# Performance work log

Measured on AMD Instinct MI355X. Metric: run time of the kernel, lower is better.

The kernel has to match this reference:

```python
import jax, jax.numpy as jnp
import numpy as np

B, L, D_MODEL, H, HD, FD = 1, 1024, 1024, 16, 64, 64
EPS = 1e-12

def setup_inputs() -> dict:
    key = jax.random.key(0)
    ks = jax.random.split(key, 7)
    s = 1.0 / np.sqrt(D_MODEL)
    return {
        'x': jax.random.normal(ks[0], (B, L, D_MODEL), jnp.float32),
        'Wq': jax.random.normal(ks[1], (D_MODEL, H * HD), jnp.float32) * s,
        'Wk': jax.random.normal(ks[2], (D_MODEL, H * HD), jnp.float32) * s,
        'Wv': jax.random.normal(ks[3], (D_MODEL, H * HD), jnp.float32) * s,
        'Wo': jax.random.normal(ks[4], (H * HD, D_MODEL), jnp.float32) * s,
        'Kq': jax.random.normal(ks[5], (H, HD, FD), jnp.float32) * (1.0 / np.sqrt(HD)),
        'Kk': jax.random.normal(ks[6], (H, HD, FD), jnp.float32) * (1.0 / np.sqrt(HD)),
    }

def _heads(t):
    # (b, l, h*d) -> (b, h, l, d)
    b, l, _ = t.shape
    return t.reshape(b, l, H, HD).transpose(0, 2, 1, 3)

def _feature_map(t, K):
    # UntiedHeadEinsumMLP (no skip) + SoftmaxDim with temp=1.0
    f = jnp.einsum('hdf,bhld->bhlf', K, t)
    feats = jnp.concatenate([jax.nn.softmax(f, axis=-1), jax.nn.softmax(-f, axis=-1)], axis=-1)
    return jnp.maximum(feats, EPS)  # clamp(min=eps)

def reference(x, Wq, Wk, Wv, Wo, Kq, Kk):
    q = _heads(x @ Wq)  # b h l d
    k = _heads(x @ Wk)
    v = _heads(x @ Wv)
    qf = _feature_map(q, Kq)  # b h l 2f
    kf = _feature_map(k, Kk)  # b h l 2f
    # causal linear attention: o_t = phi(q_t) . sum_{s<=t} phi(k_s) v_s^T, normalized
    kv = jnp.cumsum(kf[:, :, :, None, :] * v[..., None], axis=2)  # b h l d 2f
    o = jnp.einsum('bhlf,bhldf->bhld', qf, kv)
    z = jnp.einsum('bhlf,bhlf->bhl', qf, jnp.cumsum(kf, axis=2)) + EPS
    o = o / z[..., None]
    y = o.transpose(0, 2, 1, 3).reshape(x.shape[0], x.shape[1], H * HD)
    return y @ Wo
```

## Files before the change

kernel.cpp:

```cpp
#include <hip/hip_runtime.h>
#include <hip/hip_bf16.h>


#define NH 16
#define NC 16

using short8 = __attribute__((ext_vector_type(8))) short;
using f32x4  = __attribute__((ext_vector_type(4))) float;
typedef const __attribute__((address_space(1))) char* gptr1;
typedef __attribute__((address_space(3))) char* lptr3;

static __device__ __forceinline__ unsigned short bf16bits(float x) {
    __hip_bfloat16 h = __float2bfloat16(x);
    return __builtin_bit_cast(unsigned short, h);
}
static __device__ __forceinline__ float b2f(unsigned short u) {
    return __builtin_bit_cast(float, (unsigned int)u << 16);
}
#define SWZ(row, cb) ((cb) ^ (((row) & 7) << 4))

template<int RS>
static __device__ __forceinline__ short8 ldfrag(const char* buf, int row, int kelem) {
    return *(const short8*)(buf + row * RS + SWZ(row, kelem * 2));
}

__global__ __launch_bounds__(256) void prep(const float* __restrict__ x,
                                            const float* __restrict__ w0,
                                            const float* __restrict__ w1,
                                            const float* __restrict__ w2,
                                            const float* __restrict__ w3,
                                            const float* __restrict__ Kq,
                                            const float* __restrict__ Kk,
                                            __hip_bfloat16* __restrict__ xb,
                                            __hip_bfloat16* __restrict__ d0,
                                            __hip_bfloat16* __restrict__ d1,
                                            __hip_bfloat16* __restrict__ d2,
                                            __hip_bfloat16* __restrict__ d3,
                                            __hip_bfloat16* __restrict__ KqT,
                                            __hip_bfloat16* __restrict__ KkT) {
    const int z = blockIdx.z;
    const int tid = threadIdx.x;
    if (z < 4) {
        const float* src = (z == 0) ? w0 : (z == 1) ? w1 : (z == 2) ? w2 : w3;
        __hip_bfloat16* dst = (z == 0) ? d0 : (z == 1) ? d1 : (z == 2) ? d2 : d3;
        __shared__ float tile[64][68];
        const int bx = blockIdx.x * 64, by = blockIdx.y * 64;
#pragma unroll
        for (int j = 0; j < 4; j++) {
            const int idx = j * 256 + tid;
            const int kr = idx >> 4, c4 = idx & 15;
            float4 v = *(const float4*)&src[(size_t)(by + kr) * 1024 + bx + c4 * 4];
            *(float4*)&tile[kr][c4 * 4] = v;
        }
        __syncthreads();
        const int n = tid >> 2, k0 = (tid & 3) * 16;
        unsigned short* drow = (unsigned short*)dst + (size_t)(bx + n) * 1024 + by + k0;
#pragma unroll
        for (int q = 0; q < 4; q++) {
            ushort4 o;
            o.x = bf16bits(tile[k0 + q * 4 + 0][n]);
            o.y = bf16bits(tile[k0 + q * 4 + 1][n]);
            o.z = bf16bits(tile[k0 + q * 4 + 2][n]);
            o.w = bf16bits(tile[k0 + q * 4 + 3][n]);
            *(ushort4*)(drow + q * 4) = o;
        }
    } else if (z == 4) {
        const int blk = blockIdx.y * 16 + blockIdx.x;
#pragma unroll
        for (int j = 0; j < 4; j++) {
            const int i = blk * 4096 + j * 1024 + tid * 4;
            float4 v = *(const float4*)(x + i);
            ushort4 o;
            o.x = bf16bits(v.x); o.y = bf16bits(v.y); o.z = bf16bits(v.z); o.w = bf16bits(v.w);
            *(ushort4*)((unsigned short*)xb + i) = o;
        }
    } else {
        const int flat = blockIdx.y * 16 + blockIdx.x;
        if (flat >= 32) return;
        const int h = flat & 15;
        const float* S = (flat >> 4) ? Kk : Kq;
        __hip_bfloat16* D = (flat >> 4) ? KkT : KqT;
        __shared__ float t[64][65];
#pragma unroll
        for (int j = 0; j < 16; j++) {
            int e = tid + j * 256, r = e >> 6, c = e & 63;
            t[r][c] = S[h * 4096 + r * 64 + c];
        }
        __syncthreads();
#pragma unroll
        for (int j = 0; j < 16; j++) {
            int e = tid + j * 256, r = e >> 6, c = e & 63;
            D[h * 4096 + r * 64 + c] = __float2bfloat16(t[c][r]);
        }
    }
}

__global__ __launch_bounds__(256) void qkv_feat(const __hip_bfloat16* __restrict__ A,
                                                const __hip_bfloat16* __restrict__ B0,
                                                const __hip_bfloat16* __restrict__ B1,
                                                const __hip_bfloat16* __restrict__ B2,
                                                const __hip_bfloat16* __restrict__ KqT,
                                                const __hip_bfloat16* __restrict__ KkT,
                                                __hip_bfloat16* __restrict__ qf,
                                                __hip_bfloat16* __restrict__ kf,
                                                __hip_bfloat16* __restrict__ kfT,
                                                __hip_bfloat16* __restrict__ VT) {
    __shared__ __align__(16) char smem[49152];
    const int tid = threadIdx.x;
    const int bm = blockIdx.y * 128;
    const int which = blockIdx.x >> 4;
    const int h = blockIdx.x & 15;
    const __hip_bfloat16* B = (which == 0) ? B0 : (which == 1) ? B1 : B2;
    const int bn = h * 64;
    const int wid = tid >> 6, lane = tid & 63;
    const int g = lane >> 4, r16 = lane & 15;
    const char* Ab = (const char*)A;
    const char* Bb = (const char*)B;
    f32x4 acc[2][4] = {};

#define QKV_STAGE(dstA, dstB, kbyte)                                                                   \
    do {                                                                                               \
        _Pragma("unroll") for (int it = 0; it < 4; it++) {                                             \
            const int off = it * 4096 + tid * 16;                                                      \
            const int row = off >> 7, cb = off & 127;                                                  \
            __builtin_amdgcn_global_load_lds((gptr1)(Ab + (size_t)(bm + row) * 2048 + (kbyte) + SWZ(row, cb)), \
                                             (lptr3)((dstA) + it * 4096 + wid * 1024), 16, 0, 0);      \
        }                                                                                              \
        _Pragma("unroll") for (int it = 0; it < 2; it++) {                                             \
            const int off = it * 4096 + tid * 16;                                                      \
            const int row = off >> 7, cb = off & 127;                                                  \
            __builtin_amdgcn_global_load_lds((gptr1)(Bb + (size_t)(bn + row) * 2048 + (kbyte) + SWZ(row, cb)), \
                                             (lptr3)((dstB) + it * 4096 + wid * 1024), 16, 0, 0);      \
        }                                                                                              \
    } while (0)

    QKV_STAGE(smem, smem + 32768, 0);
    for (int kt = 0; kt < 16; kt++) {
        char* Ac = smem + ((kt & 1) ? 16384 : 0);
        char* Bc = smem + 32768 + ((kt & 1) ? 8192 : 0);
        if (kt < 15) {
            char* An = smem + ((kt & 1) ? 0 : 16384);
            char* Bn = smem + 32768 + ((kt & 1) ? 0 : 8192);
            QKV_STAGE(An, Bn, (kt + 1) * 128);
            asm volatile("s_waitcnt vmcnt(6)" ::: "memory");
        } else {
            asm volatile("s_waitcnt vmcnt(0)" ::: "memory");
        }
        __builtin_amdgcn_s_barrier();
#pragma unroll
        for (int ks = 0; ks < 2; ks++) {
            short8 af[2], bfr[4];
#pragma unroll
            for (int m = 0; m < 2; m++)
                af[m] = ldfrag<128>(Ac, wid * 32 + m * 16 + r16, ks * 32 + g * 8);
#pragma unroll
            for (int n = 0; n < 4; n++)
                bfr[n] = ldfrag<128>(Bc, n * 16 + r16, ks * 32 + g * 8);
#pragma unroll
            for (int m = 0; m < 2; m++)
#pragma unroll
// ... 37 lines not shown
        for (int it = 0; it < 2; it++) {
            const int off = it * 4096 + tid * 16;
            const int row = off >> 7, cb = off & 127;
            __builtin_amdgcn_global_load_lds((gptr1)(KTp + (size_t)(h * 64 + row) * 128 + SWZ(row, cb)),
                                             (lptr3)(smem + it * 4096 + wid * 1024), 16, 0, 0);
        }
    }
    __syncthreads();

    f32x4 fr[2][4] = {};
#pragma unroll
    for (int ks = 0; ks < 2; ks++) {
        short8 af[2], bfr[4];
#pragma unroll
        for (int m = 0; m < 2; m++)
            af[m] = ldfrag<128>(XS, wid * 32 + m * 16 + r16, ks * 32 + g * 8);
#pragma unroll
        for (int n = 0; n < 4; n++)
            bfr[n] = ldfrag<128>(smem, n * 16 + r16, ks * 32 + g * 8);
#pragma unroll
        for (int m = 0; m < 2; m++)
#pragma unroll
            for (int n = 0; n < 4; n++)
                fr[m][n] = __builtin_amdgcn_mfma_f32_16x16x32_bf16(af[m], bfr[n], fr[m][n], 0, 0, 0);
    }
    if (kside) __syncthreads();

    char* ft = smem;
    __hip_bfloat16* feat = kside ? kf : qf;
#pragma unroll
    for (int m = 0; m < 2; m++)
#pragma unroll
        for (int i = 0; i < 4; i++) {
            const int row = wid * 32 + m * 16 + g * 4 + i;
            float m1 = fr[m][0][i], m2 = -fr[m][0][i];
#pragma unroll
            for (int n = 1; n < 4; n++) {
                m1 = fmaxf(m1, fr[m][n][i]);
                m2 = fmaxf(m2, -fr[m][n][i]);
            }
#pragma unroll
            for (int off = 8; off; off >>= 1) {
                m1 = fmaxf(m1, __shfl_xor(m1, off));
                m2 = fmaxf(m2, __shfl_xor(m2, off));
            }
            float e1[4], e2[4], s1 = 0.f, s2 = 0.f;
#pragma unroll
            for (int n = 0; n < 4; n++) {
                e1[n] = __expf(fr[m][n][i] - m1);  s1 += e1[n];
                e2[n] = __expf(-fr[m][n][i] - m2); s2 += e2[n];
            }
#pragma unroll
            for (int off = 8; off; off >>= 1) {
                s1 += __shfl_xor(s1, off);
                s2 += __shfl_xor(s2, off);
            }
            const float i1 = 1.f / s1, i2 = 1.f / s2;
            __hip_bfloat16* fo = feat + ((size_t)(h * 1024 + bm + row)) * 128;
#pragma unroll
            for (int n = 0; n < 4; n++) {
                const int col = n * 16 + r16;
                unsigned short v1 = bf16bits(fmaxf(e1[n] * i1, 1e-12f));
                unsigned short v2 = bf16bits(fmaxf(e2[n] * i2, 1e-12f));
                *(unsigned short*)(fo + col) = v1;
                *(unsigned short*)(fo + col + 64) = v2;
                if (kside) {
                    *(unsigned short*)(ft + col * 256 + SWZ(col, row * 2)) = v1;
                    *(unsigned short*)(ft + (col + 64) * 256 + SWZ(col + 64, row * 2)) = v2;
                }
            }
        }
    if (kside) {
        __syncthreads();
#pragma unroll
        for (int j = 0; j < 8; j++) {
            const int off = (tid + j * 256) * 16;
            const int row = off >> 8, cb = off & 255;
            short8 v = *(const short8*)(ft + row * 256 + SWZ(row, cb));
            *(short8*)((char*)kfT + ((size_t)(h * 128 + row) * 1024 + bm) * 2 + cb) = v;
        }
    }
}

__global__ __launch_bounds__(256) void chunk_sums_mfma(const __hip_bfloat16* __restrict__ kfT,
                                                       const __hip_bfloat16* __restrict__ VT,
                                                       __hip_bfloat16* __restrict__ Scb,
                                                       float* __restrict__ ksum) {
    const int h = blockIdx.y, c = blockIdx.x, l0 = c * 64;
    __shared__ __align__(16) char VTs[64 * 128];
    __shared__ __align__(16) char KTs[128 * 128];
    const int tid = threadIdx.x, lane = tid & 63, wid = tid >> 6;
    const int r16 = lane & 15, g = lane >> 4;
#pragma unroll
    for (int it = 0; it < 2; it++) {
        const int off = it * 4096 + tid * 16;
        const int row = off >> 7, cb = off & 127;
        __builtin_amdgcn_global_load_lds((gptr1)((const char*)VT + ((size_t)(h * 64 + row) * 1024 + l0) * 2 + SWZ(row, cb)),
                                         (lptr3)(VTs + it * 4096 + wid * 1024), 16, 0, 0);
    }
#pragma unroll
    for (int it = 0; it < 4; it++) {
        const int off = it * 4096 + tid * 16;
        const int row = off >> 7, cb = off & 127;
        __builtin_amdgcn_global_load_lds((gptr1)((const char*)kfT + ((size_t)(h * 128 + row) * 1024 + l0) * 2 + SWZ(row, cb)),
                                         (lptr3)(KTs + it * 4096 + wid * 1024), 16, 0, 0);
    }
    __syncthreads();
    f32x4 acc[8] = {};
#pragma unroll
    for (int ks = 0; ks < 2; ks++) {
        short8 a = ldfrag<128>(VTs, wid * 16 + r16, ks * 32 + g * 8);
#pragma unroll
        for (int n = 0; n < 8; n++) {
            short8 b = ldfrag<128>(KTs, n * 16 + r16, ks * 32 + g * 8);
            acc[n] = __builtin_amdgcn_mfma_f32_16x16x32_bf16(a, b, acc[n], 0, 0, 0);
        }
    }
    unsigned short* o = (unsigned short*)Scb + (size_t)(h * NC + c) * 8192;
#pragma unroll
    for (int n = 0; n < 8; n++)
#pragma unroll
        for (int i = 0; i < 4; i++)
            o[(wid * 16 + g * 4 + i) * 128 + n * 16 + r16] = bf16bits(acc[n][i]);
    if (tid < 128) {
        float s = 0.f;
#pragma unroll 8
        for (int t = 0; t < 64; t++)
            s += b2f(*(const unsigned short*)(KTs + tid * 128 + SWZ(tid, t * 2)));
        ksum[(size_t)(h * NC + c) * 128 + tid] = s;
    }
}

__global__ __launch_bounds__(256) void prefix_scan(const __hip_bfloat16* __restrict__ Scb,
                                                   __hip_bfloat16* __restrict__ Sp,
                                                   const float* __restrict__ ksum,
                                                   float* __restrict__ kp) {
    const int h = blockIdx.x, eb = blockIdx.y, tid = threadIdx.x;
#pragma unroll
    for (int j = 0; j < 4; j++) {
        const int e = eb * 1024 + tid + j * 256;
        float v[NC];
#pragma unroll
        for (int c = 0; c < NC; c++)
            v[c] = b2f(((const unsigned short*)Scb)[(size_t)(h * NC + c) * 8192 + e]);
        float run = 0.f;
#pragma unroll
        for (int c = 0; c < NC; c++) {
            Sp[(size_t)(h * NC + c) * 8192 + e] = __float2bfloat16(run);
            run += v[c];
        }
    }
    if (eb == 0 && tid < 128) {
        float run = 0.f;
#pragma unroll
        for (int c = 0; c < NC; c++) {
            const size_t idx = (size_t)(h * NC + c) * 128 + tid;
            kp[idx] = run;
            run += ksum[idx];
        }
    }
}

__global__ __launch_bounds__(256) void chunk_out_mfma(const __hip_bfloat16* __restrict__ qf,
                                                      const __hip_bfloat16* __restrict__ kf,
                                                      const __hip_bfloat16* __restrict__ VT,
                                                      const __hip_bfloat16* __restrict__ Sp,
                                                      const float* __restrict__ kp,
                                                      __hip_bfloat16* __restrict__ Y) {
    const int h = blockIdx.y, c = blockIdx.x, l0 = c * 64;
    __shared__ __align__(16) char QF[64 * 256];
    __shared__ __align__(16) char KF[64 * 256];
    __shared__ __align__(16) char SP[64 * 256];
    __shared__ __align__(16) char VTs[64 * 128];
    __shared__ __align__(16) char AM[64 * 128];
    __shared__ float zi[64];
    __shared__ float invz[64];
    const int tid = threadIdx.x, lane = tid & 63, wid = tid >> 6;
    const int r16 = lane & 15, g = lane >> 4;

#pragma unroll
    for (int it = 0; it < 4; it++) {
        const int off = it * 4096 + wid * 1024 + lane * 16;
        const int row = off >> 8, cb = off & 255;
        const int sw = SWZ(row, cb);
        __builtin_amdgcn_global_load_lds((gptr1)((const char*)qf + ((size_t)(h * 1024 + l0 + row)) * 256 + sw),
                                         (lptr3)(QF + it * 4096 + wid * 1024), 16, 0, 0);
        __builtin_amdgcn_global_load_lds((gptr1)((const char*)kf + ((size_t)(h * 1024 + l0 + row)) * 256 + sw),
                                         (lptr3)(KF + it * 4096 + wid * 1024), 16, 0, 0);
        __builtin_amdgcn_global_load_lds((gptr1)((const char*)Sp + ((size_t)((h * NC + c) * 64 + row)) * 256 + sw),
                                         (lptr3)(SP + it * 4096 + wid * 1024), 16, 0, 0);
    }
#pragma unroll
    for (int it = 0; it < 2; it++) {
        const int off = it * 4096 + wid * 1024 + lane * 16;
        const int row = off >> 7, cb = off & 127;
        __builtin_amdgcn_global_load_lds((gptr1)((const char*)VT + ((size_t)(h * 64 + row) * 1024 + l0) * 2 + SWZ(row, cb)),
                                         (lptr3)(VTs + it * 4096 + wid * 1024), 16, 0, 0);
    }
    __syncthreads();

    f32x4 a4[4] = {};
#pragma unroll
    for (int ks = 0; ks < 4; ks++) {
        short8 a = ldfrag<256>(QF, wid * 16 + r16, ks * 32 + g * 8);
#pragma unroll
        for (int n = 0; n < 4; n++) {
            short8 bb = ldfrag<256>(KF, n * 16 + r16, ks * 32 + g * 8);
            a4[n] = __builtin_amdgcn_mfma_f32_16x16x32_bf16(a, bb, a4[n], 0, 0, 0);
        }
    }
    const int rowl = wid * 16 + g * 4;
#pragma unroll
    for (int i = 0; i < 4; i++) {
        float r = 0.f;
#pragma unroll
        for (int n = 0; n < 4; n++) {
            const int col = n * 16 + r16;
            float v = (col <= rowl + i) ? a4[n][i] : 0.f;
            a4[n][i] = v;
            r += v;
        }
#pragma unroll
        for (int off = 8; off; off >>= 1) r += __shfl_xor(r, off);
        if (r16 == 0) zi[rowl + i] = r;
#pragma unroll
        for (int n = 0; n < 4; n++)
            *(unsigned short*)(AM + (rowl + i) * 128 + SWZ(rowl + i, (n * 16 + r16) * 2)) = bf16bits(a4[n][i]);
    }
    __syncthreads();

    if (tid < 64) {
        float z = zi[tid] + 1e-12f;
        const float* kpp = kp + (size_t)(h * NC + c) * 128;
#pragma unroll 8
        for (int f = 0; f < 128; f++)
            z += b2f(*(const unsigned short*)(QF + tid * 256 + SWZ(tid, f * 2))) * kpp[f];
        invz[tid] = 1.f / z;
    }

    f32x4 o4[4] = {};
#pragma unroll
    for (int ks = 0; ks < 2; ks++) {
        short8 a = ldfrag<128>(AM, wid * 16 + r16, ks * 32 + g * 8);
#pragma unroll
        for (int n = 0; n < 4; n++) {
            short8 bb = ldfrag<128>(VTs, n * 16 + r16, ks * 32 + g * 8);
            o4[n] = __builtin_amdgcn_mfma_f32_16x16x32_bf16(a, bb, o4[n], 0, 0, 0);
        }
    }
#pragma unroll
    for (int ks = 0; ks < 4; ks++) {
        short8 a = ldfrag<256>(QF, wid * 16 + r16, ks * 32 + g * 8);
#pragma unroll
        for (int n = 0; n < 4; n++) {
            short8 bb = ldfrag<256>(SP, n * 16 + r16, ks * 32 + g * 8);
            o4[n] = __builtin_amdgcn_mfma_f32_16x16x32_bf16(a, bb, o4[n], 0, 0, 0);
        }
    }
    __syncthreads();
#pragma unroll
    for (int n = 0; n < 4; n++)
#pragma unroll
        for (int i = 0; i < 4; i++) {
            const int row = rowl + i, col = n * 16 + r16;
            Y[((size_t)(l0 + row)) * 1024 + h * 64 + col] = __float2bfloat16(o4[n][i] * invz[row]);
        }
}

__global__ __launch_bounds__(256) void gemm_final(const __hip_bfloat16* __restrict__ A,
                                                  const __hip_bfloat16* __restrict__ B,
                                                  float* __restrict__ C) {
    __shared__ __align__(16) char smem[32768];
    const int tid = threadIdx.x;
    const int bm = blockIdx.y * 64, bn = blockIdx.x * 64;
    const int wid = tid >> 6, lane = tid & 63;
    const int g = lane >> 4, r16 = lane & 15;
    const int wr = wid >> 1, wc = wid & 1;
    const char* Ab = (const char*)A;
    const char* Bb = (const char*)B;
    f32x4 acc[2][2] = {};

#define FIN_STAGE(dstA, dstB, kbyte)                                                                   \
    do {                                                                                               \
        _Pragma("unroll") for (int it = 0; it < 2; it++) {                                             \
            const int off = it * 4096 + tid * 16;                                                      \
            const int row = off >> 7, cb = off & 127;                                                  \
            __builtin_amdgcn_global_load_lds((gptr1)(Ab + (size_t)(bm + row) * 2048 + (kbyte) + SWZ(row, cb)), \
                                             (lptr3)((dstA) + it * 4096 + wid * 1024), 16, 0, 0);      \
            __builtin_amdgcn_global_load_lds((gptr1)(Bb + (size_t)(bn + row) * 2048 + (kbyte) + SWZ(row, cb)), \
                                             (lptr3)((dstB) + it * 4096 + wid * 1024), 16, 0, 0);      \
        }                                                                                              \
    } while (0)

    FIN_STAGE(smem, smem + 16384, 0);
    for (int kt = 0; kt < 16; kt++) {
        char* Ac = smem + ((kt & 1) ? 8192 : 0);
        char* Bc = smem + 16384 + ((kt & 1) ? 8192 : 0);
        if (kt < 15) {
            char* An = smem + ((kt & 1) ? 0 : 8192);
            char* Bn = smem + 16384 + ((kt & 1) ? 0 : 8192);
            FIN_STAGE(An, Bn, (kt + 1) * 128);
            asm volatile("s_waitcnt vmcnt(4)" ::: "memory");
        } else {
            asm volatile("s_waitcnt vmcnt(0)" ::: "memory");
        }
        __builtin_amdgcn_s_barrier();
#pragma unroll
        for (int ks = 0; ks < 2; ks++) {
            short8 af[2], bfr[2];
#pragma unroll
            for (int m = 0; m < 2; m++)
                af[m] = ldfrag<128>(Ac, wr * 32 + m * 16 + r16, ks * 32 + g * 8);
#pragma unroll
            for (int n = 0; n < 2; n++)
                bfr[n] = ldfrag<128>(Bc, wc * 32 + n * 16 + r16, ks * 32 + g * 8);
#pragma unroll
            for (int m = 0; m < 2; m++)
#pragma unroll
                for (int n = 0; n < 2; n++)
                    acc[m][n] = __builtin_amdgcn_mfma_f32_16x16x32_bf16(af[m], bfr[n], acc[m][n], 0, 0, 0);
        }
        asm volatile("s_waitcnt lgkmcnt(0)" ::: "memory");
        __builtin_amdgcn_s_barrier();
    }
#undef FIN_STAGE
#pragma unroll
    for (int m = 0; m < 2; m++)
#pragma unroll
        for (int n = 0; n < 2; n++)
#pragma unroll
            for (int i = 0; i < 4; i++) {
                const int row = bm + wr * 32 + m * 16 + g * 4 + i;
                const int col = bn + wc * 32 + n * 16 + r16;
                C[(size_t)row * 1024 + col] = acc[m][n][i];
            }
}

extern "C" void kernel_launch(void* const* d_in, const int* in_sizes, int n_in,
                              void* d_out, int out_size, void* d_ws, size_t ws_size,
                              hipStream_t stream) {
    const float* x  = (const float*)d_in[0];
    const float* Wq = (const float*)d_in[1];
    const float* Wk = (const float*)d_in[2];
    const float* Wv = (const float*)d_in[3];
    const float* Wo = (const float*)d_in[4];
    const float* Kq = (const float*)d_in[5];
    const float* Kk = (const float*)d_in[6];
    float* out = (float*)d_out;
    float* ws = (float*)d_ws;

    const size_t M1 = 1024 * 1024;
    if (ws_size < 10 * M1 * sizeof(float)) return;

    __hip_bfloat16* xb  = (__hip_bfloat16*)(ws);
    __hip_bfloat16* Wqt = (__hip_bfloat16*)(ws + M1 / 2);
    __hip_bfloat16* Wkt = (__hip_bfloat16*)(ws + 1 * M1);
    __hip_bfloat16* Wvt = (__hip_bfloat16*)(ws + 3 * M1 / 2);
    __hip_bfloat16* Wot = (__hip_bfloat16*)(ws + 2 * M1);
    __hip_bfloat16* KqT = (__hip_bfloat16*)(ws + 5 * M1 / 2);
    __hip_bfloat16* KkT = (__hip_bfloat16*)(ws + 5 * M1 / 2 + 32768);
    __hip_bfloat16* VT  = (__hip_bfloat16*)(ws + 3 * M1);
    __hip_bfloat16* qfb = (__hip_bfloat16*)(ws + 7 * M1 / 2);
    __hip_bfloat16* kfb = (__hip_bfloat16*)(ws + 9 * M1 / 2);
    __hip_bfloat16* kfT = (__hip_bfloat16*)(ws + 11 * M1 / 2);
    __hip_bfloat16* Scb = (__hip_bfloat16*)(ws + 13 * M1 / 2);
    __hip_bfloat16* Spb = (__hip_bfloat16*)(ws + 15 * M1 / 2);
    __hip_bfloat16* Yb  = (__hip_bfloat16*)(ws + 17 * M1 / 2);
    float* ksum = ws + 9 * M1;
    float* kp   = ws + 9 * M1 + 32768;

    prep<<<dim3(16, 16, 6), 256, 0, stream>>>(x, Wq, Wk, Wv, Wo, Kq, Kk,
                                              xb, Wqt, Wkt, Wvt, Wot, KqT, KkT);
    qkv_feat<<<dim3(48, 8), 256, 0, stream>>>(xb, Wqt, Wkt, Wvt, KqT, KkT, qfb, kfb, kfT, VT);
    chunk_sums_mfma<<<dim3(NC, NH), 256, 0, stream>>>(kfT, VT, Scb, ksum);
    prefix_scan<<<dim3(NH, 8), 256, 0, stream>>>(Scb, Spb, ksum, kp);
    chunk_out_mfma<<<dim3(NC, NH), 256, 0, stream>>>(qfb, kfb, VT, Spb, kp, Yb);
    gemm_final<<<dim3(16, 16), 256, 0, stream>>>(Yb, Wot, out);
}
```

Baseline: 54.83 us.

## Fuse chunk sums, prefix scan, chunk output and output GEMM into one flag-synchronized kernel

Replaces four tail kernels with a single persistent-style kernel that computes per-chunk KV sums, publishes them via release flags, and has each block sum all earlier chunks' states itself instead of a separate prefix scan. After writing Y, blocks wait on a per-row-chunk counter until all heads are done, then run the output projection tile for that chunk. This removes three launches and the Sp/kp intermediate round-trips, but adds spin-waits that rely on all 256 blocks being co-resident and repeats prefix summation work (quadratic in chunk count).

```diff
diff --git a/kernel.cpp b/kernel.cpp
--- a/kernel.cpp
+++ b/kernel.cpp
@@ -37,7 +37,8 @@
                                             __hip_bfloat16* __restrict__ d2,
                                             __hip_bfloat16* __restrict__ d3,
                                             __hip_bfloat16* __restrict__ KqT,
-                                            __hip_bfloat16* __restrict__ KkT) {
+                                            __hip_bfloat16* __restrict__ KkT,
+                                            int* __restrict__ flags) {
     const int z = blockIdx.z;
     const int tid = threadIdx.x;
     if (z < 4) {
@@ -76,6 +77,12 @@
         }
     } else {
         const int flat = blockIdx.y * 16 + blockIdx.x;
+        if (flat == 32) {
+            flags[tid] = 0;
+            if (tid < 16) flags[256 + tid] = 0;
+            return;
+        }
+        if (flat > 32) return;
         if (flat >= 32) return;
         const int h = flat & 15;
         const float* S = (flat >> 4) ? Kk : Kq;
@@ -279,101 +286,72 @@
     }
 }
 
-__global__ __launch_bounds__(256) void chunk_sums_mfma(const __hip_bfloat16* __restrict__ kfT,
-                                                       const __hip_bfloat16* __restrict__ VT,
-                                                       __hip_bfloat16* __restrict__ Scb,
-                                                       float* __restrict__ ksum) {
+__global__ __launch_bounds__(256) void tail_fused(const __hip_bfloat16* __restrict__ kfT,
+                                                  const __hip_bfloat16* __restrict__ VT,
+                                                  const __hip_bfloat16* __restrict__ qf,
+                                                  const __hip_bfloat16* __restrict__ kf,
+                                                  __hip_bfloat16* __restrict__ Scb,
+                                                  float* __restrict__ ksum,
+                                                  int* __restrict__ flags,
+                                                  __hip_bfloat16* __restrict__ Y,
+                                                  const __hip_bfloat16* __restrict__ Wot,
+                                                  float* __restrict__ out) {
+    __shared__ __align__(16) char smem[65536];
+    char* QF  = smem;
+    char* KF  = smem + 16384;
+    char* SP  = smem + 32768;
+    char* VTs = smem + 49152;
+    char* AM  = smem + 57344;
+    __shared__ float kpL[128];
+    __shared__ float zi[64], invz[64];
     const int h = blockIdx.y, c = blockIdx.x, l0 = c * 64;
-    __shared__ __align__(16) char VTs[64 * 128];
-    __shared__ __align__(16) char KTs[128 * 128];
     const int tid = threadIdx.x, lane = tid & 63, wid = tid >> 6;
     const int r16 = lane & 15, g = lane >> 4;
-#pragma unroll
-    for (int it = 0; it < 2; it++) {
-        const int off = it * 4096 + tid * 16;
-        const int row = off >> 7, cb = off & 127;
-        __builtin_amdgcn_global_load_lds((gptr1)((const char*)VT + ((size_t)(h * 64 + row) * 1024 + l0) * 2 + SWZ(row, cb)),
-                                         (lptr3)(VTs + it * 4096 + wid * 1024), 16, 0, 0);
-    }
-#pragma unroll
-    for (int it = 0; it < 4; it++) {
-        const int off = it * 4096 + tid * 16;
-        const int row = off >> 7, cb = off & 127;
-        __builtin_amdgcn_global_load_lds((gptr1)((const char*)kfT + ((size_t)(h * 128 + row) * 1024 + l0) * 2 + SWZ(row, cb)),
-                                         (lptr3)(KTs + it * 4096 + wid * 1024), 16, 0, 0);
+    int* flagsY = flags + 256;
+
+    {
+#pragma unroll
+        for (int it = 0; it < 2; it++) {
+            const int off = it * 4096 + tid * 16;
+            const int row = off >> 7, cb = off & 127;
+            __builtin_amdgcn_global_load_lds((gptr1)((const char*)VT + ((size_t)(h * 64 + row) * 1024 + l0) * 2 + SWZ(row, cb)),
+                                             (lptr3)(VTs + it * 4096 + wid * 1024), 16, 0, 0);
+        }
+#pragma unroll
+        for (int it = 0; it < 4; it++) {
+            const int off = it * 4096 + tid * 16;
+            const int row = off >> 7, cb = off & 127;
+            __builtin_amdgcn_global_load_lds((gptr1)((const char*)kfT + ((size_t)(h * 128 + row) * 1024 + l0) * 2 + SWZ(row, cb)),
+                                             (lptr3)(KF + it * 4096 + wid * 1024), 16, 0, 0);
+        }
+        __syncthreads();
+        f32x4 acc[8] = {};
+#pragma unroll
+        for (int ks = 0; ks < 2; ks++) {
+            short8 a = ldfrag<128>(VTs, wid * 16 + r16, ks * 32 + g * 8);
+#pragma unroll
+            for (int n = 0; n < 8; n++) {
+                short8 bb = ldfrag<128>(KF, n * 16 + r16, ks * 32 + g * 8);
+                acc[n] = __builtin_amdgcn_mfma_f32_16x16x32_bf16(a, bb, acc[n], 0, 0, 0);
+            }
+        }
+        unsigned short* o = (unsigned short*)Scb + (size_t)(h * NC + c) * 8192;
+#pragma unroll
+        for (int n = 0; n < 8; n++)
+#pragma unroll
+            for (int i = 0; i < 4; i++)
+                o[(wid * 16 + g * 4 + i) * 128 + n * 16 + r16] = bf16bits(acc[n][i]);
+        if (tid < 128) {
+            float s = 0.f;
+#pragma unroll 8
+            for (int t = 0; t < 64; t++)
+                s += b2f(*(const unsigned short*)(KF + tid * 128 + SWZ(tid, t * 2)));
+            ksum[(size_t)(h * NC + c) * 128 + tid] = s;
+        }
     }
     __syncthreads();
-    f32x4 acc[8] = {};
-#pragma unroll
-    for (int ks = 0; ks < 2; ks++) {
-        short8 a = ldfrag<128>(VTs, wid * 16 + r16, ks * 32 + g * 8);
-#pragma unroll
-        for (int n = 0; n < 8; n++) {
-            short8 b = ldfrag<128>(KTs, n * 16 + r16, ks * 32 + g * 8);
-            acc[n] = __builtin_amdgcn_mfma_f32_16x16x32_bf16(a, b, acc[n], 0, 0, 0);
-        }
-    }
-    unsigned short* o = (unsigned short*)Scb + (size_t)(h * NC + c) * 8192;
-#pragma unroll
-    for (int n = 0; n < 8; n++)
-#pragma unroll
-        for (int i = 0; i < 4; i++)
-            o[(wid * 16 + g * 4 + i) * 128 + n * 16 + r16] = bf16bits(acc[n][i]);
-    if (tid < 128) {
-        float s = 0.f;
-#pragma unroll 8
-        for (int t = 0; t < 64; t++)
-            s += b2f(*(const unsigned short*)(KTs + tid * 128 + SWZ(tid, t * 2)));
-        ksum[(size_t)(h * NC + c) * 128 + tid] = s;
-    }
-}
-
-__global__ __launch_bounds__(256) void prefix_scan(const __hip_bfloat16* __restrict__ Scb,
-                                                   __hip_bfloat16* __restrict__ Sp,
-                                                   const float* __restrict__ ksum,
-                                                   float* __restrict__ kp) {
-    const int h = blockIdx.x, eb = blockIdx.y, tid = threadIdx.x;
-#pragma unroll
-    for (int j = 0; j < 4; j++) {
-        const int e = eb * 1024 + tid + j * 256;
-        float v[NC];
-#pragma unroll
-        for (int c = 0; c < NC; c++)
-            v[c] = b2f(((const unsigned short*)Scb)[(size_t)(h * NC + c) * 8192 + e]);
-        float run = 0.f;
-#pragma unroll
-        for (int c = 0; c < NC; c++) {
-            Sp[(size_t)(h * NC + c) * 8192 + e] = __float2bfloat16(run);
-            run += v[c];
-        }
-    }
-    if (eb == 0 && tid < 128) {
-        float run = 0.f;
-#pragma unroll
-        for (int c = 0; c < NC; c++) {
-            const size_t idx = (size_t)(h * NC + c) * 128 + tid;
-            kp[idx] = run;
-            run += ksum[idx];
-        }
-    }
-}
-
-__global__ __launch_bounds__(256) void chunk_out_mfma(const __hip_bfloat16* __restrict__ qf,
-                                                      const __hip_bfloat16* __restrict__ kf,
-                                                      const __hip_bfloat16* __restrict__ VT,
-                                                      const __hip_bfloat16* __restrict__ Sp,
-                                                      const float* __restrict__ kp,
-                                                      __hip_bfloat16* __restrict__ Y) {
-    const int h = blockIdx.y, c = blockIdx.x, l0 = c * 64;
-    __shared__ __align__(16) char QF[64 * 256];
-    __shared__ __align__(16) char KF[64 * 256];
-    __shared__ __align__(16) char SP[64 * 256];
-    __shared__ __align__(16) char VTs[64 * 128];
-    __shared__ __align__(16) char AM[64 * 128];
-    __shared__ float zi[64];
-    __shared__ float invz[64];
-    const int tid = threadIdx.x, lane = tid & 63, wid = tid >> 6;
-    const int r16 = lane & 15, g = lane >> 4;
+    if (tid == 0)
+        __hip_atomic_store(&flags[h * NC + c], 1, __ATOMIC_RELEASE, __HIP_MEMORY_SCOPE_AGENT);
 
 #pragma unroll
     for (int it = 0; it < 4; it++) {
@@ -384,98 +362,123 @@
                                          (lptr3)(QF + it * 4096 + wid * 1024), 16, 0, 0);
         __builtin_amdgcn_global_load_lds((gptr1)((const char*)kf + ((size_t)(h * 1024 + l0 + row)) * 256 + sw),
                                          (lptr3)(KF + it * 4096 + wid * 1024), 16, 0, 0);
-        __builtin_amdgcn_global_load_lds((gptr1)((const char*)Sp + ((size_t)((h * NC + c) * 64 + row)) * 256 + sw),
-                                         (lptr3)(SP + it * 4096 + wid * 1024), 16, 0, 0);
-    }
-#pragma unroll
-    for (int it = 0; it < 2; it++) {
-        const int off = it * 4096 + wid * 1024 + lane * 16;
-        const int row = off >> 7, cb = off & 127;
-        __builtin_amdgcn_global_load_lds((gptr1)((const char*)VT + ((size_t)(h * 64 + row) * 1024 + l0) * 2 + SWZ(row, cb)),
-                                         (lptr3)(VTs + it * 4096 + wid * 1024), 16, 0, 0);
-    }
+    }
+
+    if (tid < c)
+        while (__hip_atomic_load(&flags[h * NC + tid], __ATOMIC_ACQUIRE, __HIP_MEMORY_SCOPE_AGENT) == 0) {}
     __syncthreads();
 
-    f32x4 a4[4] = {};
-#pragma unroll
-    for (int ks = 0; ks < 4; ks++) {
-        short8 a = ldfrag<256>(QF, wid * 16 + r16, ks * 32 + g * 8);
-#pragma unroll
-        for (int n = 0; n < 4; n++) {
-            short8 bb = ldfrag<256>(KF, n * 16 + r16, ks * 32 + g * 8);
-            a4[n] = __builtin_amdgcn_mfma_f32_16x16x32_bf16(a, bb, a4[n], 0, 0, 0);
-        }
-    }
-    const int rowl = wid * 16 + g * 4;
-#pragma unroll
-    for (int i = 0; i < 4; i++) {
-        float r = 0.f;
-#pragma unroll
-        for (int n = 0; n < 4; n++) {
-            const int col = n * 16 + r16;
-            float v = (col <= rowl + i) ? a4[n][i] : 0.f;
-            a4[n][i] = v;
-            r += v;
-        }
-#pragma unroll
-        for (int off = 8; off; off >>= 1) r += __shfl_xor(r, off);
-        if (r16 == 0) zi[rowl + i] = r;
+    {
+        const int e0 = tid * 32;
+        const int d = e0 >> 7, f0 = e0 & 127;
+        float a[32];
+#pragma unroll
+        for (int j = 0; j < 32; j++) a[j] = 0.f;
+        for (int cp = 0; cp < c; cp++) {
+            const unsigned short* p = (const unsigned short*)Scb + (size_t)(h * NC + cp) * 8192 + e0;
+#pragma unroll
+            for (int q = 0; q < 4; q++) {
+                short8 v = *(const short8*)(p + q * 8);
+#pragma unroll
+                for (int j = 0; j < 8; j++) a[q * 8 + j] += b2f((unsigned short)v[j]);
+            }
+        }
+#pragma unroll
+        for (int q = 0; q < 4; q++) {
+            short8 w;
+#pragma unroll
+            for (int j = 0; j < 8; j++) w[j] = (short)bf16bits(a[q * 8 + j]);
+            *(short8*)(SP + d * 256 + SWZ(d, (f0 + q * 8) * 2)) = w;
+        }
+        if (tid < 128) {
+            float s = 0.f;
+            for (int cp = 0; cp < c; cp++)
+                s += ksum[(size_t)(h * NC + cp) * 128 + tid];
+            kpL[tid] = s;
+        }
+    }
+    __syncthreads();
+
+    {
+        f32x4 a4[4] = {};
+#pragma unroll
+        for (int ks = 0; ks < 4; ks++) {
+            short8 a = ldfrag<256>(QF, wid * 16 + r16, ks * 32 + g * 8);
+#pragma unroll
+            for (int n = 0; n < 4; n++) {
+                short8 bb = ldfrag<256>(KF, n * 16 + r16, ks * 32 + g * 8);
+                a4[n] = __builtin_amdgcn_mfma_f32_16x16x32_bf16(a, bb, a4[n], 0, 0, 0);
+            }
+        }
+        const int rowl = wid * 16 + g * 4;
+#pragma unroll
+        for (int i = 0; i < 4; i++) {
+            float r = 0.f;
+#pragma unroll
+            for (int n = 0; n < 4; n++) {
+                const int col = n * 16 + r16;
+                float v = (col <= rowl + i) ? a4[n][i] : 0.f;
+                a4[n][i] = v;
+                r += v;
+            }
+#pragma unroll
+            for (int off = 8; off; off >>= 1) r += __shfl_xor(r, off);
+            if (r16 == 0) zi[rowl + i] = r;
+#pragma unroll
+            for (int n = 0; n < 4; n++)
+                *(unsigned short*)(AM + (rowl + i) * 128 + SWZ(rowl + i, (n * 16 + r16) * 2)) = bf16bits(a4[n][i]);
+        }
+        __syncthreads();
+
+        if (tid < 64) {
+            float z = zi[tid] + 1e-12f;
+#pragma unroll 8
+            for (int f = 0; f < 128; f++)
+                z += b2f(*(const unsigned short*)(QF + tid * 256 + SWZ(tid, f * 2))) * kpL[f];
+            invz[tid] = 1.f / z;
+        }
+
+        f32x4 o4[4] = {};
+#pragma unroll
+        for (int ks = 0; ks < 2; ks++) {
+            short8 a = ldfrag<128>(AM, wid * 16 + r16, ks * 32 + g * 8);
+#pragma unroll
+            for (int n = 0; n < 4; n++) {
+                short8 bb = ldfrag<128>(VTs, n * 16 + r16, ks * 32 + g * 8);
+                o4[n] = __builtin_amdgcn_mfma_f32_16x16x32_bf16(a, bb, o4[n], 0, 0, 0);
+            }
+        }
+#pragma unroll
+        for (int ks = 0; ks < 4; ks++) {
+            short8 a = ldfrag<256>(QF, wid * 16 + r16, ks * 32 + g * 8);
+#pragma unroll
+            for (int n = 0; n < 4; n++) {
+                short8 bb = ldfrag<256>(SP, n * 16 + r16, ks * 32 + g * 8);
+                o4[n] = __builtin_amdgcn_mfma_f32_16x16x32_bf16(a, bb, o4[n], 0, 0, 0);
+            }
+        }
+        __syncthreads();
 #pragma unroll
         for (int n = 0; n < 4; n++)
-            *(unsigned short*)(AM + (rowl + i) * 128 + SWZ(rowl + i, (n * 16 + r16) * 2)) = bf16bits(a4[n][i]);
+#pragma unroll
+            for (int i = 0; i < 4; i++) {
+                const int row = rowl + i, col = n * 16 + r16;
+                Y[((size_t)(l0 + row)) * 1024 + h * 64 + col] = __float2bfloat16(o4[n][i] * invz[row]);
+            }
     }
     __syncthreads();
-
-    if (tid < 64) {
-        float z = zi[tid] + 1e-12f;
-        const float* kpp = kp + (size_t)(h * NC + c) * 128;
-#pragma unroll 8
-        for (int f = 0; f < 128; f++)
-            z += b2f(*(const unsigned short*)(QF + tid * 256 + SWZ(tid, f * 2))) * kpp[f];
-        invz[tid] = 1.f / z;
-    }
-
-    f32x4 o4[4] = {};
-#pragma unroll
-    for (int ks = 0; ks < 2; ks++) {
-        short8 a = ldfrag<128>(AM, wid * 16 + r16, ks * 32 + g * 8);
-#pragma unroll
-        for (int n = 0; n < 4; n++) {
-            short8 bb = ldfrag<128>(VTs, n * 16 + r16, ks * 32 + g * 8);
-            o4[n] = __builtin_amdgcn_mfma_f32_16x16x32_bf16(a, bb, o4[n], 0, 0, 0);
-        }
-    }
-#pragma unroll
-    for (int ks = 0; ks < 4; ks++) {
-        short8 a = ldfrag<256>(QF, wid * 16 + r16, ks * 32 + g * 8);
-#pragma unroll
-        for (int n = 0; n < 4; n++) {
-            short8 bb = ldfrag<256>(SP, n * 16 + r16, ks * 32 + g * 8);
-            o4[n] = __builtin_amdgcn_mfma_f32_16x16x32_bf16(a, bb, o4[n], 0, 0, 0);
-        }
+    if (tid == 0) {
+        __hip_atomic_fetch_add(&flagsY[c], 1, __ATOMIC_RELEASE, __HIP_MEMORY_SCOPE_AGENT);
+        while (__hip_atomic_load(&flagsY[c], __ATOMIC_ACQUIRE, __HIP_MEMORY_SCOPE_AGENT) < NH) {}
     }
     __syncthreads();
-#pragma unroll
-    for (int n = 0; n < 4; n++)
-#pragma unroll
-        for (int i = 0; i < 4; i++) {
-            const int row = rowl + i, col = n * 16 + r16;
-            Y[((size_t)(l0 + row)) * 1024 + h * 64 + col] = __float2bfloat16(o4[n][i] * invz[row]);
-        }
-}
-
-__global__ __launch_bounds__(256) void gemm_final(const __hip_bfloat16* __restrict__ A,
-                                                  const __hip_bfloat16* __restrict__ B,
-                                                  float* __restrict__ C) {
-    __shared__ __align__(16) char smem[32768];
-    const int tid = threadIdx.x;
-    const int bm = blockIdx.y * 64, bn = blockIdx.x * 64;
-    const int wid = tid >> 6, lane = tid & 63;
-    const int g = lane >> 4, r16 = lane & 15;
-    const int wr = wid >> 1, wc = wid & 1;
-    const char* Ab = (const char*)A;
-    const char* Bb = (const char*)B;
-    f32x4 acc[2][2] = {};
+
+    {
+        const int bm = c * 64, bn = h * 64;
+        const int wr = wid >> 1, wc = wid & 1;
+        const char* Ab = (const char*)Y;
+        const char* Bb = (const char*)Wot;
+        f32x4 acc[2][2] = {};
 
 #define FIN_STAGE(dstA, dstB, kbyte)                                                                   \
     do {                                                                                               \
@@ -489,48 +492,49 @@
         }                                                                                              \
     } while (0)
 
-    FIN_STAGE(smem, smem + 16384, 0);
-    for (int kt = 0; kt < 16; kt++) {
-        char* Ac = smem + ((kt & 1) ? 8192 : 0);
-        char* Bc = smem + 16384 + ((kt & 1) ? 8192 : 0);
-        if (kt < 15) {
-            char* An = smem + ((kt & 1) ? 0 : 8192);
-            char* Bn = smem + 16384 + ((kt & 1) ? 0 : 8192);
-            FIN_STAGE(An, Bn, (kt + 1) * 128);
-            asm volatile("s_waitcnt vmcnt(4)" ::: "memory");
-        } else {
-            asm volatile("s_waitcnt vmcnt(0)" ::: "memory");
-        }
-        __builtin_amdgcn_s_barrier();
-#pragma unroll
-        for (int ks = 0; ks < 2; ks++) {
-            short8 af[2], bfr[2];
-#pragma unroll
-            for (int m = 0; m < 2; m++)
-                af[m] = ldfrag<128>(Ac, wr * 32 + m * 16 + r16, ks * 32 + g * 8);
+        FIN_STAGE(QF, KF, 0);
+        for (int kt = 0; kt < 16; kt++) {
+            char* Ac = QF + ((kt & 1) ? 8192 : 0);
+            char* Bc = KF + ((kt & 1) ? 8192 : 0);
+            if (kt < 15) {
+                char* An = QF + ((kt & 1) ? 0 : 8192);
+                char* Bn = KF + ((kt & 1) ? 0 : 8192);
+                FIN_STAGE(An, Bn, (kt + 1) * 128);
+                asm volatile("s_waitcnt vmcnt(4)" ::: "memory");
+            } else {
+                asm volatile("s_waitcnt vmcnt(0)" ::: "memory");
+            }
+            __builtin_amdgcn_s_barrier();
+#pragma unroll
+            for (int ks = 0; ks < 2; ks++) {
+                short8 af[2], bfr[2];
+#pragma unroll
+                for (int m = 0; m < 2; m++)
+                    af[m] = ldfrag<128>(Ac, wr * 32 + m * 16 + r16, ks * 32 + g * 8);
+#pragma unroll
+                for (int n = 0; n < 2; n++)
+                    bfr[n] = ldfrag<128>(Bc, wc * 32 + n * 16 + r16, ks * 32 + g * 8);
+#pragma unroll
+                for (int m = 0; m < 2; m++)
+#pragma unroll
+                    for (int n = 0; n < 2; n++)
+                        acc[m][n] = __builtin_amdgcn_mfma_f32_16x16x32_bf16(af[m], bfr[n], acc[m][n], 0, 0, 0);
+            }
+            asm volatile("s_waitcnt lgkmcnt(0)" ::: "memory");
+            __builtin_amdgcn_s_barrier();
+        }
+#undef FIN_STAGE
+#pragma unroll
+        for (int m = 0; m < 2; m++)
 #pragma unroll
             for (int n = 0; n < 2; n++)
-                bfr[n] = ldfrag<128>(Bc, wc * 32 + n * 16 + r16, ks * 32 + g * 8);
-#pragma unroll
-            for (int m = 0; m < 2; m++)
-#pragma unroll
-                for (int n = 0; n < 2; n++)
-                    acc[m][n] = __builtin_amdgcn_mfma_f32_16x16x32_bf16(af[m], bfr[n], acc[m][n], 0, 0, 0);
-        }
-        asm volatile("s_waitcnt lgkmcnt(0)" ::: "memory");
-        __builtin_amdgcn_s_barrier();
-    }
-#undef FIN_STAGE
-#pragma unroll
-    for (int m = 0; m < 2; m++)
-#pragma unroll
-        for (int n = 0; n < 2; n++)
-#pragma unroll
-            for (int i = 0; i < 4; i++) {
-                const int row = bm + wr * 32 + m * 16 + g * 4 + i;
-                const int col = bn + wc * 32 + n * 16 + r16;
-                C[(size_t)row * 1024 + col] = acc[m][n][i];
-            }
+#pragma unroll
+                for (int i = 0; i < 4; i++) {
+                    const int row = bm + wr * 32 + m * 16 + g * 4 + i;
+                    const int col = bn + wc * 32 + n * 16 + r16;
+                    out[(size_t)row * 1024 + col] = acc[m][n][i];
+                }
+    }
 }
 
 extern "C" void kernel_launch(void* const* d_in, const int* in_sizes, int n_in,
@@ -561,16 +565,12 @@
     __hip_bfloat16* kfb = (__hip_bfloat16*)(ws + 9 * M1 / 2);
     __hip_bfloat16* kfT = (__hip_bfloat16*)(ws + 11 * M1 / 2);
     __hip_bfloat16* Scb = (__hip_bfloat16*)(ws + 13 * M1 / 2);
-    __hip_bfloat16* Spb = (__hip_bfloat16*)(ws + 15 * M1 / 2);
-    __hip_bfloat16* Yb  = (__hip_bfloat16*)(ws + 17 * M1 / 2);
+    __hip_bfloat16* Yb  = (__hip_bfloat16*)(ws + 15 * M1 / 2);
     float* ksum = ws + 9 * M1;
-    float* kp   = ws + 9 * M1 + 32768;
+    int*   flags = (int*)(ws + 9 * M1 + 32768);
 
     prep<<<dim3(16, 16, 6), 256, 0, stream>>>(x, Wq, Wk, Wv, Wo, Kq, Kk,
-                                              xb, Wqt, Wkt, Wvt, Wot, KqT, KkT);
+                                              xb, Wqt, Wkt, Wvt, Wot, KqT, KkT, flags);
     qkv_feat<<<dim3(48, 8), 256, 0, stream>>>(xb, Wqt, Wkt, Wvt, KqT, KkT, qfb, kfb, kfT, VT);
-    chunk_sums_mfma<<<dim3(NC, NH), 256, 0, stream>>>(kfT, VT, Scb, ksum);
-    prefix_scan<<<dim3(NH, 8), 256, 0, stream>>>(Scb, Spb, ksum, kp);
-    chunk_out_mfma<<<dim3(NC, NH), 256, 0, stream>>>(qfb, kfb, VT, Spb, kp, Yb);
-    gemm_final<<<dim3(16, 16), 256, 0, stream>>>(Yb, Wot, out);
-}
+    tail_fused<<<dim3(NC, NH), 256, 0, stream>>>(kfT, VT, qfb, kfb, Scb, ksum, flags, Yb, Wot, out);
+}
```

Result: slower. 79.92 us (+45.8%).

## Fuse chunk state sums and prefix scan into one sequential pipelined kernel

Applied to the files above, without the earlier changes.

Replaces the per-chunk sum kernel and the separate prefix-scan kernel with a single kernel. Each block walks all chunks of a head sequentially, keeping the running state in registers and the running key sum in LDS, and double-buffers the next chunk's loads. This removes a kernel launch and the round trip of the per-chunk sums through global memory. In exchange the grid shrinks from 256 blocks to 32, and the chunk loop is serialized, which may leave most of the GPU idle.

```diff
diff --git a/kernel.cpp b/kernel.cpp
--- a/kernel.cpp
+++ b/kernel.cpp
@@ -279,83 +279,92 @@
     }
 }
 
-__global__ __launch_bounds__(256) void chunk_sums_mfma(const __hip_bfloat16* __restrict__ kfT,
-                                                       const __hip_bfloat16* __restrict__ VT,
-                                                       __hip_bfloat16* __restrict__ Scb,
-                                                       float* __restrict__ ksum) {
-    const int h = blockIdx.y, c = blockIdx.x, l0 = c * 64;
-    __shared__ __align__(16) char VTs[64 * 128];
-    __shared__ __align__(16) char KTs[128 * 128];
+__global__ __launch_bounds__(256) void chunk_scan(const __hip_bfloat16* __restrict__ kfT,
+                                                  const __hip_bfloat16* __restrict__ VT,
+                                                  __hip_bfloat16* __restrict__ Sp,
+                                                  float* __restrict__ kp) {
+    __shared__ __align__(16) char smem[40960];
+    __shared__ float kprun[128];
+    __shared__ float kpP[2][128];
+    const int h = blockIdx.y, dh = blockIdx.x;
     const int tid = threadIdx.x, lane = tid & 63, wid = tid >> 6;
     const int r16 = lane & 15, g = lane >> 4;
-#pragma unroll
-    for (int it = 0; it < 2; it++) {
-        const int off = it * 4096 + tid * 16;
-        const int row = off >> 7, cb = off & 127;
-        __builtin_amdgcn_global_load_lds((gptr1)((const char*)VT + ((size_t)(h * 64 + row) * 1024 + l0) * 2 + SWZ(row, cb)),
-                                         (lptr3)(VTs + it * 4096 + wid * 1024), 16, 0, 0);
-    }
-#pragma unroll
-    for (int it = 0; it < 4; it++) {
-        const int off = it * 4096 + tid * 16;
-        const int row = off >> 7, cb = off & 127;
-        __builtin_amdgcn_global_load_lds((gptr1)((const char*)kfT + ((size_t)(h * 128 + row) * 1024 + l0) * 2 + SWZ(row, cb)),
-                                         (lptr3)(KTs + it * 4096 + wid * 1024), 16, 0, 0);
-    }
-    __syncthreads();
-    f32x4 acc[8] = {};
-#pragma unroll
-    for (int ks = 0; ks < 2; ks++) {
-        short8 a = ldfrag<128>(VTs, wid * 16 + r16, ks * 32 + g * 8);
-#pragma unroll
-        for (int n = 0; n < 8; n++) {
-            short8 b = ldfrag<128>(KTs, n * 16 + r16, ks * 32 + g * 8);
-            acc[n] = __builtin_amdgcn_mfma_f32_16x16x32_bf16(a, b, acc[n], 0, 0, 0);
-        }
-    }
-    unsigned short* o = (unsigned short*)Scb + (size_t)(h * NC + c) * 8192;
-#pragma unroll
-    for (int n = 0; n < 8; n++)
-#pragma unroll
-        for (int i = 0; i < 4; i++)
-            o[(wid * 16 + g * 4 + i) * 128 + n * 16 + r16] = bf16bits(acc[n][i]);
-    if (tid < 128) {
-        float s = 0.f;
-#pragma unroll 8
-        for (int t = 0; t < 64; t++)
-            s += b2f(*(const unsigned short*)(KTs + tid * 128 + SWZ(tid, t * 2)));
-        ksum[(size_t)(h * NC + c) * 128 + tid] = s;
-    }
-}
-
-__global__ __launch_bounds__(256) void prefix_scan(const __hip_bfloat16* __restrict__ Scb,
-                                                   __hip_bfloat16* __restrict__ Sp,
-                                                   const float* __restrict__ ksum,
-                                                   float* __restrict__ kp) {
-    const int h = blockIdx.x, eb = blockIdx.y, tid = threadIdx.x;
-#pragma unroll
-    for (int j = 0; j < 4; j++) {
-        const int e = eb * 1024 + tid + j * 256;
-        float v[NC];
-#pragma unroll
-        for (int c = 0; c < NC; c++)
-            v[c] = b2f(((const unsigned short*)Scb)[(size_t)(h * NC + c) * 8192 + e]);
-        float run = 0.f;
-#pragma unroll
-        for (int c = 0; c < NC; c++) {
-            Sp[(size_t)(h * NC + c) * 8192 + e] = __float2bfloat16(run);
-            run += v[c];
-        }
-    }
-    if (eb == 0 && tid < 128) {
-        float run = 0.f;
-#pragma unroll
-        for (int c = 0; c < NC; c++) {
-            const size_t idx = (size_t)(h * NC + c) * 128 + tid;
-            kp[idx] = run;
-            run += ksum[idx];
-        }
-    }
+    if (tid < 128) kprun[tid] = 0.f;
+
+    f32x4 acc[2][2] = {};
+
+#define CS_STAGE(p, kc)                                                                                 \
+    do {                                                                                                \
+        char* bufp = smem + (p) * 20480;                                                                \
+        {                                                                                               \
+            const int off = tid * 16;                                                                   \
+            const int row = off >> 7, cb = off & 127;                                                   \
+            __builtin_amdgcn_global_load_lds((gptr1)((const char*)VT + ((size_t)(h * 64 + dh * 32 + row) * 1024 + (kc) * 64) * 2 + SWZ(row, cb)), \
+                                             (lptr3)(bufp + wid * 1024), 16, 0, 0);                     \
+        }                                                                                               \
+        _Pragma("unroll") for (int it = 0; it < 4; it++) {                                              \
+            const int off = it * 4096 + tid * 16;                                                       \
+            const int row = off >> 7, cb = off & 127;                                                   \
+            __builtin_amdgcn_global_load_lds((gptr1)((const char*)kfT + ((size_t)(h * 128 + row) * 1024 + (kc) * 64) * 2 + SWZ(row, cb)), \
+                                             (lptr3)(bufp + 4096 + it * 4096 + wid * 1024), 16, 0, 0);  \
+        }                                                                                               \
+    } while (0)
+
+    CS_STAGE(0, 0);
+    for (int c = 0; c < NC; c++) {
+        char* VTc = smem + (c & 1) * 20480;
+        char* KTc = VTc + 4096;
+        if (c + 1 < NC) {
+            CS_STAGE((c + 1) & 1, c + 1);
+            asm volatile("s_waitcnt vmcnt(5)" ::: "memory");
+        } else {
+            asm volatile("s_waitcnt vmcnt(0)" ::: "memory");
+        }
+        __builtin_amdgcn_s_barrier();
+
+        unsigned short* SpO = (unsigned short*)Sp + (size_t)(h * NC + c) * 8192;
+#pragma unroll
+        for (int mt = 0; mt < 2; mt++)
+#pragma unroll
+            for (int nt = 0; nt < 2; nt++)
+#pragma unroll
+                for (int i = 0; i < 4; i++) {
+                    const int d = dh * 32 + mt * 16 + g * 4 + i;
+                    const int f = wid * 32 + nt * 16 + r16;
+                    SpO[d * 128 + f] = bf16bits(acc[mt][nt][i]);
+                }
+        if (dh == 0 && tid < 128) kp[(size_t)(h * NC + c) * 128 + tid] = kprun[tid];
+
+#pragma unroll
+        for (int ks = 0; ks < 2; ks++) {
+            short8 af[2];
+#pragma unroll
+            for (int mt = 0; mt < 2; mt++)
+                af[mt] = ldfrag<128>(VTc, mt * 16 + r16, ks * 32 + g * 8);
+#pragma unroll
+            for (int nt = 0; nt < 2; nt++) {
+                short8 bb = ldfrag<128>(KTc, wid * 32 + nt * 16 + r16, ks * 32 + g * 8);
+#pragma unroll
+                for (int mt = 0; mt < 2; mt++)
+                    acc[mt][nt] = __builtin_amdgcn_mfma_f32_16x16x32_bf16(af[mt], bb, acc[mt][nt], 0, 0, 0);
+            }
+        }
+        {
+            const int f = tid & 127, half = tid >> 7;
+            float s = 0.f;
+#pragma unroll
+            for (int j = 0; j < 4; j++) {
+                short8 v = ldfrag<128>(KTc, f, half * 32 + j * 8);
+#pragma unroll
+                for (int e = 0; e < 8; e++) s += b2f((unsigned short)v[e]);
+            }
+            kpP[half][f] = s;
+        }
+        asm volatile("s_waitcnt lgkmcnt(0)" ::: "memory");
+        __builtin_amdgcn_s_barrier();
+        if (tid < 128) kprun[tid] += kpP[0][tid] + kpP[1][tid];
+    }
+#undef CS_STAGE
 }
 
 __global__ __launch_bounds__(256) void chunk_out_mfma(const __hip_bfloat16* __restrict__ qf,
@@ -560,17 +569,14 @@
     __hip_bfloat16* qfb = (__hip_bfloat16*)(ws + 7 * M1 / 2);
     __hip_bfloat16* kfb = (__hip_bfloat16*)(ws + 9 * M1 / 2);
     __hip_bfloat16* kfT = (__hip_bfloat16*)(ws + 11 * M1 / 2);
-    __hip_bfloat16* Scb = (__hip_bfloat16*)(ws + 13 * M1 / 2);
-    __hip_bfloat16* Spb = (__hip_bfloat16*)(ws + 15 * M1 / 2);
-    __hip_bfloat16* Yb  = (__hip_bfloat16*)(ws + 17 * M1 / 2);
-    float* ksum = ws + 9 * M1;
-    float* kp   = ws + 9 * M1 + 32768;
+    __hip_bfloat16* Spb = (__hip_bfloat16*)(ws + 13 * M1 / 2);
+    __hip_bfloat16* Yb  = (__hip_bfloat16*)(ws + 15 * M1 / 2);
+    float* kp = ws + 9 * M1;
 
     prep<<<dim3(16, 16, 6), 256, 0, stream>>>(x, Wq, Wk, Wv, Wo, Kq, Kk,
                                               xb, Wqt, Wkt, Wvt, Wot, KqT, KkT);
     qkv_feat<<<dim3(48, 8), 256, 0, stream>>>(xb, Wqt, Wkt, Wvt, KqT, KkT, qfb, kfb, kfT, VT);
-    chunk_sums_mfma<<<dim3(NC, NH), 256, 0, stream>>>(kfT, VT, Scb, ksum);
-    prefix_scan<<<dim3(NH, 8), 256, 0, stream>>>(Scb, Spb, ksum, kp);
+    chunk_scan<<<dim3(2, NH), 256, 0, stream>>>(kfT, VT, Spb, kp);
     chunk_out_mfma<<<dim3(NC, NH), 256, 0, stream>>>(qfb, kfb, VT, Spb, kp, Yb);
     gemm_final<<<dim3(16, 16), 256, 0, stream>>>(Yb, Wot, out);
 }
```

Result: slower. 64.61 us (+17.8%).

## Fuse chunk prefix scan into chunk output kernel, recomputing prefixes per block

Applied to the files above, without the earlier changes.

Removes the separate prefix_scan launch and its intermediate Sp/kp buffers. Each chunk_out block now sums the bf16 chunk states of all earlier chunks (and the ksum vectors) directly into LDS before its MFMA work. This saves one kernel launch and a global round-trip, but adds redundant reads that grow with chunk index, so late chunks read up to 15 states, and the load imbalance across blocks rises.

```diff
diff --git a/kernel.cpp b/kernel.cpp
--- a/kernel.cpp
+++ b/kernel.cpp
@@ -328,48 +328,19 @@
     }
 }
 
-__global__ __launch_bounds__(256) void prefix_scan(const __hip_bfloat16* __restrict__ Scb,
-                                                   __hip_bfloat16* __restrict__ Sp,
-                                                   const float* __restrict__ ksum,
-                                                   float* __restrict__ kp) {
-    const int h = blockIdx.x, eb = blockIdx.y, tid = threadIdx.x;
-#pragma unroll
-    for (int j = 0; j < 4; j++) {
-        const int e = eb * 1024 + tid + j * 256;
-        float v[NC];
-#pragma unroll
-        for (int c = 0; c < NC; c++)
-            v[c] = b2f(((const unsigned short*)Scb)[(size_t)(h * NC + c) * 8192 + e]);
-        float run = 0.f;
-#pragma unroll
-        for (int c = 0; c < NC; c++) {
-            Sp[(size_t)(h * NC + c) * 8192 + e] = __float2bfloat16(run);
-            run += v[c];
-        }
-    }
-    if (eb == 0 && tid < 128) {
-        float run = 0.f;
-#pragma unroll
-        for (int c = 0; c < NC; c++) {
-            const size_t idx = (size_t)(h * NC + c) * 128 + tid;
-            kp[idx] = run;
-            run += ksum[idx];
-        }
-    }
-}
-
-__global__ __launch_bounds__(256) void chunk_out_mfma(const __hip_bfloat16* __restrict__ qf,
-                                                      const __hip_bfloat16* __restrict__ kf,
-                                                      const __hip_bfloat16* __restrict__ VT,
-                                                      const __hip_bfloat16* __restrict__ Sp,
-                                                      const float* __restrict__ kp,
-                                                      __hip_bfloat16* __restrict__ Y) {
+__global__ __launch_bounds__(256) void chunk_out_pf(const __hip_bfloat16* __restrict__ qf,
+                                                    const __hip_bfloat16* __restrict__ kf,
+                                                    const __hip_bfloat16* __restrict__ VT,
+                                                    const __hip_bfloat16* __restrict__ Scb,
+                                                    const float* __restrict__ ksum,
+                                                    __hip_bfloat16* __restrict__ Y) {
     const int h = blockIdx.y, c = blockIdx.x, l0 = c * 64;
     __shared__ __align__(16) char QF[64 * 256];
     __shared__ __align__(16) char KF[64 * 256];
     __shared__ __align__(16) char SP[64 * 256];
     __shared__ __align__(16) char VTs[64 * 128];
     __shared__ __align__(16) char AM[64 * 128];
+    __shared__ float kpL[128];
     __shared__ float zi[64];
     __shared__ float invz[64];
     const int tid = threadIdx.x, lane = tid & 63, wid = tid >> 6;
@@ -384,8 +355,6 @@
                                          (lptr3)(QF + it * 4096 + wid * 1024), 16, 0, 0);
         __builtin_amdgcn_global_load_lds((gptr1)((const char*)kf + ((size_t)(h * 1024 + l0 + row)) * 256 + sw),
                                          (lptr3)(KF + it * 4096 + wid * 1024), 16, 0, 0);
-        __builtin_amdgcn_global_load_lds((gptr1)((const char*)Sp + ((size_t)((h * NC + c) * 64 + row)) * 256 + sw),
-                                         (lptr3)(SP + it * 4096 + wid * 1024), 16, 0, 0);
     }
 #pragma unroll
     for (int it = 0; it < 2; it++) {
@@ -394,6 +363,36 @@
         __builtin_amdgcn_global_load_lds((gptr1)((const char*)VT + ((size_t)(h * 64 + row) * 1024 + l0) * 2 + SWZ(row, cb)),
                                          (lptr3)(VTs + it * 4096 + wid * 1024), 16, 0, 0);
     }
+
+    {
+        const int e0 = tid * 32;
+        const int d = e0 >> 7, f0 = e0 & 127;
+        float a[32];
+#pragma unroll
+        for (int j = 0; j < 32; j++) a[j] = 0.f;
+        for (int cp = 0; cp < c; cp++) {
+            const unsigned short* p = (const unsigned short*)Scb + (size_t)(h * NC + cp) * 8192 + e0;
+#pragma unroll
+            for (int q = 0; q < 4; q++) {
+                short8 v = *(const short8*)(p + q * 8);
+#pragma unroll
+                for (int j = 0; j < 8; j++) a[q * 8 + j] += b2f((unsigned short)v[j]);
+            }
+        }
+#pragma unroll
+        for (int q = 0; q < 4; q++) {
+            short8 w;
+#pragma unroll
+            for (int j = 0; j < 8; j++) w[j] = (short)bf16bits(a[q * 8 + j]);
+            *(short8*)(SP + d * 256 + SWZ(d, (f0 + q * 8) * 2)) = w;
+        }
+        if (tid < 128) {
+            float s = 0.f;
+            for (int cp = 0; cp < c; cp++)
+                s += ksum[(size_t)(h * NC + cp) * 128 + tid];
+            kpL[tid] = s;
+        }
+    }
     __syncthreads();
 
     f32x4 a4[4] = {};
@@ -428,10 +427,9 @@
 
     if (tid < 64) {
         float z = zi[tid] + 1e-12f;
-        const float* kpp = kp + (size_t)(h * NC + c) * 128;
 #pragma unroll 8
         for (int f = 0; f < 128; f++)
-            z += b2f(*(const unsigned short*)(QF + tid * 256 + SWZ(tid, f * 2))) * kpp[f];
+            z += b2f(*(const unsigned short*)(QF + tid * 256 + SWZ(tid, f * 2))) * kpL[f];
         invz[tid] = 1.f / z;
     }
 
@@ -561,16 +559,13 @@
     __hip_bfloat16* kfb = (__hip_bfloat16*)(ws + 9 * M1 / 2);
     __hip_bfloat16* kfT = (__hip_bfloat16*)(ws + 11 * M1 / 2);
     __hip_bfloat16* Scb = (__hip_bfloat16*)(ws + 13 * M1 / 2);
-    __hip_bfloat16* Spb = (__hip_bfloat16*)(ws + 15 * M1 / 2);
-    __hip_bfloat16* Yb  = (__hip_bfloat16*)(ws + 17 * M1 / 2);
+    __hip_bfloat16* Yb  = (__hip_bfloat16*)(ws + 15 * M1 / 2);
     float* ksum = ws + 9 * M1;
-    float* kp   = ws + 9 * M1 + 32768;
 
     prep<<<dim3(16, 16, 6), 256, 0, stream>>>(x, Wq, Wk, Wv, Wo, Kq, Kk,
                                               xb, Wqt, Wkt, Wvt, Wot, KqT, KkT);
     qkv_feat<<<dim3(48, 8), 256, 0, stream>>>(xb, Wqt, Wkt, Wvt, KqT, KkT, qfb, kfb, kfT, VT);
     chunk_sums_mfma<<<dim3(NC, NH), 256, 0, stream>>>(kfT, VT, Scb, ksum);
-    prefix_scan<<<dim3(NH, 8), 256, 0, stream>>>(Scb, Spb, ksum, kp);
-    chunk_out_mfma<<<dim3(NC, NH), 256, 0, stream>>>(qfb, kfb, VT, Spb, kp, Yb);
+    chunk_out_pf<<<dim3(NC, NH), 256, 0, stream>>>(qfb, kfb, VT, Scb, ksum, Yb);
     gemm_final<<<dim3(16, 16), 256, 0, stream>>>(Yb, Wot, out);
 }
```

Result: slower. 58.42 us (+6.5%).
